# Optimization experiments

Measured on AMD Instinct MI355X. Metric: run time of the kernel, lower is better.

Reference implementation:

```python
import jax, jax.numpy as jnp
import numpy as np

B = 64        # batch
V1 = 4096     # nodes, layer 1 (D)
V2 = 1024     # nodes after pool/4
DF = 8        # input features (DFeat)
K1 = 25       # Chebyshev order layer 1
K2 = 25       # Chebyshev order layer 2
F1 = 32       # CL1_F
F2 = 64       # CL2_F
FC1F = 512    # FC1_F
FC2F = 10     # FC2_F
E1 = 65536    # nnz of L1
E2 = 16384    # nnz of L2
FC1Fin = F2 * (V1 // 16)  # 16384


def setup_inputs() -> dict:
    key = jax.random.key(0)
    ks = jax.random.split(key, 16)
    x = jax.random.normal(ks[0], (B, V1, DF), jnp.float32)
    L1_rows = jax.random.randint(ks[1], (E1,), 0, V1, dtype=jnp.int32)
    L1_cols = jax.random.randint(ks[2], (E1,), 0, V1, dtype=jnp.int32)
    # small values keep the order-25 Chebyshev recursion numerically tame
    L1_vals = jax.random.normal(ks[3], (E1,), jnp.float32) * 0.05
    L2_rows = jax.random.randint(ks[4], (E2,), 0, V2, dtype=jnp.int32)
    L2_cols = jax.random.randint(ks[5], (E2,), 0, V2, dtype=jnp.int32)
    L2_vals = jax.random.normal(ks[6], (E2,), jnp.float32) * 0.05

    def glorot(k, shape, fin, fout):
        s = np.sqrt(2.0 / (fin + fout)).astype(np.float32)
        return jax.random.uniform(k, shape, jnp.float32, -s, s)

    cl1_w = glorot(ks[7], (F1, K1 * DF), K1, F1)
    cl1_b = jnp.zeros((F1,), jnp.float32)
    cl2_w = glorot(ks[8], (F2, K2 * F1), K2 * F1, F2)
    cl2_b = jnp.zeros((F2,), jnp.float32)
    fc1_w = glorot(ks[9], (FC1F, FC1Fin), FC1Fin, FC1F)
    fc1_b = jnp.zeros((FC1F,), jnp.float32)
    fc2_w = glorot(ks[10], (FC2F, FC1F), FC1F, FC2F)
    fc2_b = jnp.zeros((FC2F,), jnp.float32)
    return dict(x=x, L1_rows=L1_rows, L1_cols=L1_cols, L1_vals=L1_vals,
                L2_rows=L2_rows, L2_cols=L2_cols, L2_vals=L2_vals,
                cl1_w=cl1_w, cl1_b=cl1_b, cl2_w=cl2_w, cl2_b=cl2_b,
                fc1_w=fc1_w, fc1_b=fc1_b, fc2_w=fc2_w, fc2_b=fc2_b)


def _cheb_conv(x, rows, cols, vals, W, b, K):
    """Chebyshev graph conv. x: [B, V, Fin]; sparse L as COO edge lists."""
    Bb, V, Fin = x.shape
    x0 = x.transpose(1, 2, 0).reshape(V, Fin * Bb)  # [V, Fin*B]

    def spmm(y):  # sparse [V,V] @ dense [V, C]
        return jax.ops.segment_sum(vals[:, None] * y[cols], rows, num_segments=V)

    x1 = spmm(x0)

    def step(carry, _):
        xm2, xm1 = carry
        xk = 2.0 * spmm(xm1) - xm2
        return (xm1, xk), xk

    _, rest = jax.lax.scan(step, (x0, x1), None, length=K - 2)
    stack = jnp.concatenate([x0[None], x1[None], rest], axis=0)  # [K, V, Fin*B]
    # [K,V,Fin,B] -> [B,V,Fin,K] -> [B*V, Fin*K], matching torch layout
    feat = stack.reshape(K, V, Fin, Bb).transpose(3, 1, 2, 0).reshape(Bb * V, Fin * K)
    out = feat @ W.T + b
    return out.reshape(Bb, V, -1)


def _max_pool(x, p):
    Bb, V, F = x.shape
    return x.reshape(Bb, V // p, p, F).max(axis=2)


def reference(x, L1_rows, L1_cols, L1_vals, L2_rows, L2_cols, L2_vals,
              cl1_w, cl1_b, cl2_w, cl2_b, fc1_w, fc1_b, fc2_w, fc2_b):
    h = _cheb_conv(x, L1_rows, L1_cols, L1_vals, cl1_w, cl1_b, K1)
    h = jax.nn.relu(h)
    h = _max_pool(h, 4)                                   # [B, V/4, F1]
    h = _cheb_conv(h, L2_rows, L2_cols, L2_vals, cl2_w, cl2_b, K2)
    h = jax.nn.relu(h)
    h = _max_pool(h, 4)                                   # [B, V/16, F2]
    h = h.reshape(-1, FC1Fin)
    h = jax.nn.relu(h @ fc1_w.T + fc1_b)
    # dropout treated as identity (eval mode / d=0)
    return h @ fc2_w.T + fc2_b                            # [B, FC2F]
```

## Files before the change

### kernel.cpp

```cpp
#include <hip/hip_runtime.h>
#include <hip/hip_fp16.h>

#define B_    64
#define V1_   4096
#define V2_   1024
#define DF_   8
#define K_    25
#define NP_   13
#define F1_   32
#define F2_   64
#define FC1F_ 512
#define FC2F_ 10
#define E1_   65536
#define E2_   16384
#define C1_   512
#define C2_   2048
#define FCIN_ 16384

typedef short bf16x8 __attribute__((ext_vector_type(8)));
typedef float f32x4  __attribute__((ext_vector_type(4)));

#define FMA_MIX_LO(acc, qv, gv) \
    asm("v_fma_mix_f32 %0, %1, %2, %0 op_sel:[1,0,0] op_sel_hi:[1,1,0]" \
        : "+v"(acc) : "v"(qv), "v"(gv))
#define FMA_MIX_HI(acc, qv, gv) \
    asm("v_fma_mix_f32 %0, %1, %2, %0 op_sel:[1,1,0] op_sel_hi:[1,1,0]" \
        : "+v"(acc) : "v"(qv), "v"(gv))

__device__ __forceinline__ unsigned short f2bf(float x) {
    unsigned u = __float_as_uint(x);
    u += 0x7FFFu + ((u >> 16) & 1u);
    return (unsigned short)(u >> 16);
}
__device__ __forceinline__ float h2f_lo(unsigned u) {
    return __half2float(__ushort_as_half((unsigned short)(u & 0xFFFFu)));
}
__device__ __forceinline__ float h2f_hi(unsigned u) {
    return __half2float(__ushort_as_half((unsigned short)(u >> 16)));
}

__global__ __launch_bounds__(256) void k_transpose_rm(const float* __restrict__ x,
                                                      unsigned* __restrict__ XP,
                                                      unsigned* __restrict__ stk0) {
    __shared__ float tsh[DF_][B_][16];
    const int t = threadIdx.x;
    const int v0 = blockIdx.x * 16;
    for (int rep = 0; rep < 4; ++rep) {
        int idx = rep*256 + t;
        int b = idx >> 4, vv = idx & 15;
        const float4* p = (const float4*)&x[((size_t)b*V1_ + v0 + vv)*DF_];
        float4 a0 = p[0], a1 = p[1];
        tsh[0][b][vv]=a0.x; tsh[1][b][vv]=a0.y; tsh[2][b][vv]=a0.z; tsh[3][b][vv]=a0.w;
        tsh[4][b][vv]=a1.x; tsh[5][b][vv]=a1.y; tsh[6][b][vv]=a1.z; tsh[7][b][vv]=a1.w;
    }
    __syncthreads();
    for (int rep = 0; rep < 16; ++rep) {
        int idx = rep*256 + t;
        int c2 = idx & 255, vv = idx >> 8;
        int c = c2*2, fin = c >> 6, b = c & 63;
        float xa = tsh[fin][b][vv], xb = tsh[fin][b+1][vv];
        __half2 hh = __floats2half2_rn(xa, xb);
        XP[(size_t)(v0+vv)*256 + c2]   = *(const unsigned*)&hh;
        stk0[(size_t)(v0+vv)*256 + c2] = (unsigned)f2bf(xa) | ((unsigned)f2bf(xb) << 16);
    }
}

__global__ __launch_bounds__(256) void k_count(const int* __restrict__ rows, int E,
                                               int* __restrict__ cnt) {
    int e = blockIdx.x*256 + threadIdx.x;
    if (e < E) atomicAdd(&cnt[rows[e]], 1);
}

__global__ __launch_bounds__(256) void k_scan(const int* __restrict__ cnt, int V,
                                              int* __restrict__ offs, int* __restrict__ cursor) {
    __shared__ int psum[256];
    int t = threadIdx.x;
    int chunk = V >> 8;
    int lo = t*chunk;
    int s = 0;
    for (int i = lo; i < lo+chunk; ++i) s += (cnt[i] + 3) & ~3;
    psum[t] = s;
    __syncthreads();
    for (int off = 1; off < 256; off <<= 1) {
        int val = (t >= off) ? psum[t-off] : 0;
        __syncthreads();
        psum[t] += val;
        __syncthreads();
    }
    int run = (t == 0) ? 0 : psum[t-1];
    for (int i = lo; i < lo+chunk; ++i) {
        offs[i] = run; cursor[i] = run;
        run += (cnt[i] + 3) & ~3;
    }
    if (t == 255) offs[V] = run;
}

__global__ __launch_bounds__(256) void k_scatter(const int* __restrict__ rows,
                                                 const int* __restrict__ cols,
                                                 const float* __restrict__ vals, int E,
                                                 int shift,
                                                 int* __restrict__ cursor,
                                                 unsigned* __restrict__ ep) {
    int e = blockIdx.x*256 + threadIdx.x;
    if (e < E) {
        int p = atomicAdd(&cursor[rows[e]], 1);
        unsigned hv = (unsigned)__half_as_ushort(__float2half(vals[e]));
        ep[p] = (hv << 16) | ((unsigned)cols[e] << shift);
    }
}

__global__ __launch_bounds__(512) void k_dcheb1(int k,
        const unsigned short* __restrict__ Xsrc,
        unsigned short* __restrict__ Xown,
        unsigned short* __restrict__ stk16,
        const int* __restrict__ offs,
        const unsigned* __restrict__ ep) {
    const int t = threadIdx.x;
    const int lane = t & 63;
    const int v = blockIdx.x*8 + (t >> 6);
    const int e0 = offs[v], e1 = offs[v+1];
    const unsigned loff = (unsigned)lane * 16u;
    float acc[8];
#pragma unroll
    for (int j = 0; j < 8; ++j) acc[j] = 0.f;
    const char* srcb = (const char*)Xsrc;

    for (int e = e0; e < e1; e += 4) {
        const uint4 q = *(const uint4*)&ep[e];
        const uint4 g0 = *(const uint4*)(srcb + ((q.x & 0xFFFFu)*1024u + loff));
        const uint4 g1 = *(const uint4*)(srcb + ((q.y & 0xFFFFu)*1024u + loff));
        const uint4 g2 = *(const uint4*)(srcb + ((q.z & 0xFFFFu)*1024u + loff));
        const uint4 g3 = *(const uint4*)(srcb + ((q.w & 0xFFFFu)*1024u + loff));
        FMA_MIX_LO(acc[0], q.x, g0.x); FMA_MIX_HI(acc[1], q.x, g0.x);
        FMA_MIX_LO(acc[2], q.x, g0.y); FMA_MIX_HI(acc[3], q.x, g0.y);
        FMA_MIX_LO(acc[4], q.x, g0.z); FMA_MIX_HI(acc[5], q.x, g0.z);
        FMA_MIX_LO(acc[6], q.x, g0.w); FMA_MIX_HI(acc[7], q.x, g0.w);
        FMA_MIX_LO(acc[0], q.y, g1.x); FMA_MIX_HI(acc[1], q.y, g1.x);
        FMA_MIX_LO(acc[2], q.y, g1.y); FMA_MIX_HI(acc[3], q.y, g1.y);
        FMA_MIX_LO(acc[4], q.y, g1.z); FMA_MIX_HI(acc[5], q.y, g1.z);
        FMA_MIX_LO(acc[6], q.y, g1.w); FMA_MIX_HI(acc[7], q.y, g1.w);
        FMA_MIX_LO(acc[0], q.z, g2.x); FMA_MIX_HI(acc[1], q.z, g2.x);
        FMA_MIX_LO(acc[2], q.z, g2.y); FMA_MIX_HI(acc[3], q.z, g2.y);
        FMA_MIX_LO(acc[4], q.z, g2.z); FMA_MIX_HI(acc[5], q.z, g2.z);
        FMA_MIX_LO(acc[6], q.z, g2.w); FMA_MIX_HI(acc[7], q.z, g2.w);
        FMA_MIX_LO(acc[0], q.w, g3.x); FMA_MIX_HI(acc[1], q.w, g3.x);
        FMA_MIX_LO(acc[2], q.w, g3.y); FMA_MIX_HI(acc[3], q.w, g3.y);
        FMA_MIX_LO(acc[4], q.w, g3.z); FMA_MIX_HI(acc[5], q.w, g3.z);
        FMA_MIX_LO(acc[6], q.w, g3.w); FMA_MIX_HI(acc[7], q.w, g3.w);
    }

    float xn[8];
    if (k > 1) {
        const uint4 old = *(const uint4*)((const char*)Xown + ((size_t)v*1024 + loff));
        xn[0] = fmaf(2.f, acc[0], -h2f_lo(old.x));
        xn[1] = fmaf(2.f, acc[1], -h2f_hi(old.x));
        xn[2] = fmaf(2.f, acc[2], -h2f_lo(old.y));
        xn[3] = fmaf(2.f, acc[3], -h2f_hi(old.y));
        xn[4] = fmaf(2.f, acc[4], -h2f_lo(old.z));
        xn[5] = fmaf(2.f, acc[5], -h2f_hi(old.z));
        xn[6] = fmaf(2.f, acc[6], -h2f_lo(old.w));
        xn[7] = fmaf(2.f, acc[7], -h2f_hi(old.w));
    } else {
#pragma unroll
        for (int j = 0; j < 8; ++j) xn[j] = acc[j];
    }

    uint4 hp;
    { __half2 h0 = __floats2half2_rn(xn[0], xn[1]); hp.x = *(const unsigned*)&h0;
      __half2 h1 = __floats2half2_rn(xn[2], xn[3]); hp.y = *(const unsigned*)&h1;
      __half2 h2 = __floats2half2_rn(xn[4], xn[5]); hp.z = *(const unsigned*)&h2;
      __half2 h3 = __floats2half2_rn(xn[6], xn[7]); hp.w = *(const unsigned*)&h3; }
    *(uint4*)((char*)Xown + ((size_t)v*1024 + loff)) = hp;

    uint4 bp;
    bp.x = (unsigned)f2bf(xn[0]) | ((unsigned)f2bf(xn[1]) << 16);
    bp.y = (unsigned)f2bf(xn[2]) | ((unsigned)f2bf(xn[3]) << 16);
    bp.z = (unsigned)f2bf(xn[4]) | ((unsigned)f2bf(xn[5]) << 16);
    bp.w = (unsigned)f2bf(xn[6]) | ((unsigned)f2bf(xn[7]) << 16);
    *(uint4*)((char*)stk16 + (((size_t)k*V1_ + v)*1024 + loff)) = bp;
}

template<int FIN, int F>
__global__ __launch_bounds__(256) void k_wprep(const float* __restrict__ W,
                                               unsigned short* __restrict__ Wb) {
    int idx = blockIdx.x*256 + threadIdx.x;
    int kk  = idx & 7;
    int f   = (idx >> 3) % F;
    int g   = (idx >> 3) / F % 4;
    int fin = idx / (8*F*4);
    int k = g*8 + kk;
    Wb[idx] = (k < K_) ? f2bf(W[(size_t)f*(FIN*K_) + fin*K_ + k]) : 0;
}

__global__ __launch_bounds__(256) void k_gemm1b(const unsigned short* __restrict__ stk16,
                                                const unsigned short* __restrict__ Wb,
                                                const float* __restrict__ bias,
                                                float* __restrict__ X0T2) {
    const int t = threadIdx.x, lane = t & 63, wave = t >> 6;
    const int v2 = blockIdx.x*4 + wave;
    const int m = lane & 15, g = lane >> 4;
    int kbase[8];
#pragma unroll
    for (int j = 0; j < 8; ++j) {
        int kq = g*8 + j; if (kq > 24) kq = 24;
        kbase[j] = kq * (V1_*C1_);
    }
    float bv[2] = { bias[m], bias[16+m] };
    f32x4 pool[4][2];

    for (int vv = 0; vv < 4; ++vv) {
        const int v = v2*4 + vv;
        f32x4 acc[4][2];
#pragma unroll
        for (int mt = 0; mt < 4; ++mt)
#pragma unroll
            for (int ft = 0; ft < 2; ++ft) acc[mt][ft] = (f32x4){0.f,0.f,0.f,0.f};

        for (int fin = 0; fin < DF_; ++fin) {
            const int cbase = v*C1_ + fin*64 + m;
            const bf16x8 bw0 = *(const bf16x8*)&Wb[((fin*4+g)*F1_ + m)*8];
            const bf16x8 bw1 = *(const bf16x8*)&Wb[((fin*4+g)*F1_ + 16 + m)*8];
#pragma unroll
            for (int mt = 0; mt < 4; ++mt) {
                unsigned short au[8];
#pragma unroll
                for (int j = 0; j < 8; ++j)
                    au[j] = stk16[(size_t)(kbase[j] + cbase + mt*16)];
                bf16x8 a;
                __builtin_memcpy(&a, au, 16);
                acc[mt][0] = __builtin_amdgcn_mfma_f32_16x16x32_bf16(a, bw0, acc[mt][0], 0,0,0);
                acc[mt][1] = __builtin_amdgcn_mfma_f32_16x16x32_bf16(a, bw1, acc[mt][1], 0,0,0);
            }
        }
#pragma unroll
        for (int mt = 0; mt < 4; ++mt)
#pragma unroll
            for (int ft = 0; ft < 2; ++ft) {
                if (vv == 0) pool[mt][ft] = acc[mt][ft];
                else {
#pragma unroll
                    for (int j = 0; j < 4; ++j)
                        pool[mt][ft][j] = fmaxf(pool[mt][ft][j], acc[mt][ft][j]);
                }
            }
    }

#pragma unroll
    for (int mt = 0; mt < 4; ++mt)
#pragma unroll
        for (int ft = 0; ft < 2; ++ft)
#pragma unroll
            for (int j = 0; j < 4; ++j) {
                float mx = fmaxf(pool[mt][ft][j] + bv[ft], 0.f);
                int b = mt*16 + g*4 + j;
                int f = ft*16 + m;
                X0T2[(size_t)(f*64+b)*V2_ + v2] = mx;
            }
}

template<int V, int THREADS, int MINW>
__global__ __launch_bounds__(THREADS, MINW) void k_cheb2(
        const float* __restrict__ X0T,
        const int* __restrict__ offs,
        const unsigned* __restrict__ ep,
        unsigned* __restrict__ stk) {
    constexpr int RPT = V / THREADS;
    __shared__ uint2 buf[2*V];
    const int c0 = blockIdx.x*4;
    const int t = threadIdx.x;
    int e0r[RPT], e1r[RPT];
    unsigned tlo[RPT][4];
    unsigned* __restrict__ pl[4];
#pragma unroll
    for (int j = 0; j < 4; ++j) pl[j] = stk + (size_t)(c0+j)*NP_*V;

#pragma unroll
    for (int r = 0; r < RPT; ++r) {
        const int v = r*THREADS + t;
        e0r[r] = offs[v]; e1r[r] = offs[v+1];
        float xj[4];
#pragma unroll
        for (int j = 0; j < 4; ++j) {
            xj[j] = X0T[(size_t)(c0+j)*V + v];
            tlo[r][j] = f2bf(xj[j]);
        }
        __half2 ha = __floats2half2_rn(xj[0], xj[1]);
        __half2 hb = __floats2half2_rn(xj[2], xj[3]);
        buf[v] = make_uint2(*(const unsigned*)&ha, *(const unsigned*)&hb);
    }
    __syncthreads();

    auto step = [&](const uint2* __restrict__ src, uint2* __restrict__ dst,
                    bool first, bool last, int plane) {
#pragma unroll
        for (int r = 0; r < RPT; ++r) {
            const int v = r*THREADS + t;
            float acc[4][4];
#pragma unroll
            for (int j = 0; j < 4; ++j)
#pragma unroll
                for (int i = 0; i < 4; ++i) acc[j][i] = 0.f;
            const int ee0 = e0r[r], ee1 = e1r[r];
            uint4 q = *(const uint4*)&ep[ee0];
            for (int e = ee0; e < ee1; e += 4) {
                const uint4 qn = *(const uint4*)&ep[e + 4];
                const uint2 g0 = *(const uint2*)((const char*)src + (q.x & 0xFFFFu));
                const uint2 g1 = *(const uint2*)((const char*)src + (q.y & 0xFFFFu));
                const uint2 g2 = *(const uint2*)((const char*)src + (q.z & 0xFFFFu));
                const uint2 g3 = *(const uint2*)((const char*)src + (q.w & 0xFFFFu));
                FMA_MIX_LO(acc[0][0], q.x, g0.x); FMA_MIX_HI(acc[1][0], q.x, g0.x);
                FMA_MIX_LO(acc[2][0], q.x, g0.y); FMA_MIX_HI(acc[3][0], q.x, g0.y);
                FMA_MIX_LO(acc[0][1], q.y, g1.x); FMA_MIX_HI(acc[1][1], q.y, g1.x);
                FMA_MIX_LO(acc[2][1], q.y, g1.y); FMA_MIX_HI(acc[3][1], q.y, g1.y);
                FMA_MIX_LO(acc[0][2], q.z, g2.x); FMA_MIX_HI(acc[1][2], q.z, g2.x);
                FMA_MIX_LO(acc[2][2], q.z, g2.y); FMA_MIX_HI(acc[3][2], q.z, g2.y);
                FMA_MIX_LO(acc[0][3], q.w, g3.x); FMA_MIX_HI(acc[1][3], q.w, g3.x);
                FMA_MIX_LO(acc[2][3], q.w, g3.y); FMA_MIX_HI(acc[3][3], q.w, g3.y);
                q = qn;
            }
            float gs[4];
#pragma unroll
            for (int j = 0; j < 4; ++j)
                gs[j] = (acc[j][0]+acc[j][1])+(acc[j][2]+acc[j][3]);
            float xn[4];
            if (first) {
#pragma unroll
                for (int j = 0; j < 4; ++j) xn[j] = gs[j];
            } else {
                const uint2 old = dst[v];
                xn[0] = fmaf(2.f, gs[0], -h2f_lo(old.x));
                xn[1] = fmaf(2.f, gs[1], -h2f_hi(old.x));
                xn[2] = fmaf(2.f, gs[2], -h2f_lo(old.y));
                xn[3] = fmaf(2.f, gs[3], -h2f_hi(old.y));
            }
            if (!last) {
                __half2 ha = __floats2half2_rn(xn[0], xn[1]);
                __half2 hb = __floats2half2_rn(xn[2], xn[3]);
                dst[v] = make_uint2(*(const unsigned*)&ha, *(const unsigned*)&hb);
            }
            unsigned h[4];
#pragma unroll
            for (int j = 0; j < 4; ++j) h[j] = f2bf(xn[j]);
            if (plane < 0) {
#pragma unroll
                for (int j = 0; j < 4; ++j) tlo[r][j] = h[j];
            } else {
#pragma unroll
                for (int j = 0; j < 4; ++j)
                    pl[j][(size_t)plane*V + v] = tlo[r][j] | (h[j] << 16);
            }
        }
        __syncthreads();
    };

    step(buf, buf + V, true, false, 0);
    for (int k = 2; k < 24; k += 2) {
        step(buf + V, buf, false, false, -1);
        step(buf, buf + V, false, false, (k + 1) >> 1);
    }
    step(buf + V, buf, false, true, -1);

#pragma unroll
    for (int r = 0; r < RPT; ++r) {
        const int v = r*THREADS + t;
#pragma unroll
        for (int j = 0; j < 4; ++j)
            pl[j][(size_t)12*V + v] = tlo[r][j];
    }
}

__global__ __launch_bounds__(256) void k_gemm2(const unsigned* __restrict__ STK,
                                               const unsigned short* __restrict__ Wb,
                                               const float* __restrict__ bias,
                                               float* __restrict__ FCINT) {
    const int t = threadIdx.x, lane = t & 63, wave = t >> 6;
    const int b = blockIdx.x;
    const int v0 = blockIdx.y*128 + wave*32;
    const int m = lane & 15, g = lane >> 4;
    int offp[4];
#pragma unroll
    for (int p = 0; p < 4; ++p) {
        int pl = 4*g + p; if (pl > 12) pl = 12;
        offp[p] = pl*V2_ + v0 + m;
    }

    f32x4 acc[2][4];
#pragma unroll
    for (int mt = 0; mt < 2; ++mt)
#pragma unroll
        for (int ft = 0; ft < 4; ++ft) acc[mt][ft] = (f32x4){0.f,0.f,0.f,0.f};

#pragma unroll 4
    for (int fin = 0; fin < F1_; ++fin) {
        const unsigned* sp = STK + (size_t)(fin*64 + b)*(NP_*V2_);
        unsigned ua[4], ub[4];
#pragma unroll
        for (int p = 0; p < 4; ++p) { ua[p] = sp[offp[p]]; ub[p] = sp[offp[p] + 16]; }
        bf16x8 a0, a1;
        __builtin_memcpy(&a0, ua, 16);
        __builtin_memcpy(&a1, ub, 16);
#pragma unroll
        for (int ft = 0; ft < 4; ++ft) {
            const bf16x8 bw = *(const bf16x8*)&Wb[((fin*4+g)*F2_ + ft*16 + m)*8];
            acc[0][ft] = __builtin_amdgcn_mfma_f32_16x16x32_bf16(a0, bw, acc[0][ft], 0,0,0);
            acc[1][ft] = __builtin_amdgcn_mfma_f32_16x16x32_bf16(a1, bw, acc[1][ft], 0,0,0);
        }
    }
#pragma unroll
    for (int mt = 0; mt < 2; ++mt)
#pragma unroll
        for (int ft = 0; ft < 4; ++ft) {
            f32x4 a = acc[mt][ft];
            float mx = fmaxf(fmaxf(a[0],a[1]), fmaxf(a[2],a[3])) + bias[ft*16 + m];
            mx = fmaxf(mx, 0.f);
            int v2 = blockIdx.y*32 + wave*8 + mt*4 + g;
            FCINT[((size_t)v2*64 + ft*16 + m)*64 + b] = mx;
        }
}

__global__ __launch_bounds__(256) void k_fc1_init(const float* __restrict__ bias,
                                                  float* __restrict__ O) {
    int idx = blockIdx.x*256 + threadIdx.x;
    O[idx] = bias[idx & (FC1F_-1)];
}

__global__ __launch_bounds__(256) void k_fc1(const float* __restrict__ AT,
                                             const float* __restrict__ W,
                                             float* __restrict__ O) {
    const int t = threadIdx.x;
    const int b = t & 63;
    const int jq = __builtin_amdgcn_readfirstlane(t >> 6);
    const int j0 = blockIdx.x*32 + jq*8;
    const int i0 = blockIdx.y*1024;
    float acc[8] = {};
    for (int i = i0; i < i0 + 1024; i += 4) {
        float a0 = AT[(size_t)(i+0)*64 + b];
        float a1 = AT[(size_t)(i+1)*64 + b];
        float a2 = AT[(size_t)(i+2)*64 + b];
        float a3 = AT[(size_t)(i+3)*64 + b];
#pragma unroll
        for (int jj = 0; jj < 8; ++jj) {
            const float* wp = &W[(size_t)(j0+jj)*FCIN_ + i];
            acc[jj] = fmaf(a0, wp[0], acc[jj]);
            acc[jj] = fmaf(a1, wp[1], acc[jj]);
            acc[jj] = fmaf(a2, wp[2], acc[jj]);
            acc[jj] = fmaf(a3, wp[3], acc[jj]);
        }
    }
#pragma unroll
    for (int jj = 0; jj < 8; ++jj)
        atomicAdd(&O[b*FC1F_ + j0 + jj], acc[jj]);
}

__global__ void k_fc2(const float* __restrict__ O1, const float* __restrict__ W2,
                      const float* __restrict__ b2, float* __restrict__ out) {
    int c = blockIdx.x;
    int b = threadIdx.x;
    float s = b2[c];
    for (int j = 0; j < FC1F_; ++j)
        s = fmaf(fmaxf(O1[b*FC1F_ + j], 0.f), W2[c*FC1F_ + j], s);
    out[b*FC2F_ + c] = s;
}

extern "C" void kernel_launch(void* const* d_in, const int* in_sizes, int n_in,
                              void* d_out, int out_size, void* d_ws, size_t ws_size,
                              hipStream_t stream) {
    const float* x   = (const float*)d_in[0];
    const int*   l1r = (const int*)d_in[1];
    const int*   l1c = (const int*)d_in[2];
    const float* l1v = (const float*)d_in[3];
    const int*   l2r = (const int*)d_in[4];
    const int*   l2c = (const int*)d_in[5];
    const float* l2v = (const float*)d_in[6];
    const float* w1  = (const float*)d_in[7];
    const float* b1  = (const float*)d_in[8];
    const float* w2  = (const float*)d_in[9];
    const float* b2  = (const float*)d_in[10];
    const float* fw1 = (const float*)d_in[11];
    const float* fb1 = (const float*)d_in[12];
    const float* fw2 = (const float*)d_in[13];
    const float* fb2 = (const float*)d_in[14];
    float* out = (float*)d_out;

    char* wsp = (char*)d_ws;
    size_t off = 0;
    auto alloc = [&](size_t bytes) -> void* {
        void* p = wsp + off;
        off += (bytes + 255) & ~size_t(255);
        return p;
    };
    void*     STKU  = alloc((size_t)C2_*NP_*V2_*4);
    unsigned short* stk16 = (unsigned short*)STKU;
    unsigned*       STACK = (unsigned*)STKU;
    unsigned short* XB0   = (unsigned short*)alloc((size_t)V1_*C1_*2);
    unsigned short* XB1   = (unsigned short*)alloc((size_t)V1_*C1_*2);
    float*    X0T2  = (float*)alloc((size_t)C2_*V2_*4);
    float*    FCINT = (float*)alloc((size_t)FCIN_*B_*4);
    float*    FC1O  = (float*)alloc((size_t)B_*FC1F_*4);
    unsigned short* WB1 = (unsigned short*)alloc((size_t)DF_*4*F1_*8*2);
    unsigned short* WB2 = (unsigned short*)alloc((size_t)F1_*4*F2_*8*2);
    int*      cnt1  = (int*)alloc(V1_*4);
    int*      offs1 = (int*)alloc((V1_+1)*4);
    int*      cur1  = (int*)alloc(V1_*4);
    unsigned* ep1   = (unsigned*)alloc((size_t)(E1_ + 4*V1_ + 8)*4);
    int*      cnt2  = (int*)alloc(V2_*4);
    int*      offs2 = (int*)alloc((V2_+1)*4);
    int*      cur2  = (int*)alloc(V2_*4);
    unsigned* ep2   = (unsigned*)alloc((size_t)(E2_ + 4*V2_ + 8)*4);

    hipMemsetAsync(cnt1, 0, V1_*4, stream);
    hipMemsetAsync(ep1, 0, (size_t)(E1_ + 4*V1_ + 8)*4, stream);
    hipMemsetAsync(cnt2, 0, V2_*4, stream);
    hipMemsetAsync(ep2, 0, (size_t)(E2_ + 4*V2_ + 8)*4, stream);
    hipLaunchKernelGGL(k_count,   dim3(E1_/256), dim3(256), 0, stream, l1r, E1_, cnt1);
    hipLaunchKernelGGL(k_scan,    dim3(1),       dim3(256), 0, stream, cnt1, V1_, offs1, cur1);
    hipLaunchKernelGGL(k_scatter, dim3(E1_/256), dim3(256), 0, stream, l1r, l1c, l1v, E1_, 0, cur1, ep1);
    hipLaunchKernelGGL(k_count,   dim3(E2_/256), dim3(256), 0, stream, l2r, E2_, cnt2);
    hipLaunchKernelGGL(k_scan,    dim3(1),       dim3(256), 0, stream, cnt2, V2_, offs2, cur2);
    hipLaunchKernelGGL(k_scatter, dim3(E2_/256), dim3(256), 0, stream, l2r, l2c, l2v, E2_, 3, cur2, ep2);
    hipLaunchKernelGGL((k_wprep<DF_,F1_>), dim3(DF_*4*F1_*8/256), dim3(256), 0, stream, w1, WB1);
    hipLaunchKernelGGL((k_wprep<F1_,F2_>), dim3(F1_*4*F2_*8/256), dim3(256), 0, stream, w2, WB2);

    hipLaunchKernelGGL(k_transpose_rm, dim3(V1_/16), dim3(256), 0, stream,
                       x, (unsigned*)XB0, (unsigned*)stk16);
    for (int k = 1; k <= 24; ++k) {
        unsigned short* src = (k & 1) ? XB0 : XB1;
        unsigned short* own = (k & 1) ? XB1 : XB0;
        hipLaunchKernelGGL(k_dcheb1, dim3(V1_/8), dim3(512), 0, stream,
                           k, src, own, stk16, offs1, ep1);
    }
    hipLaunchKernelGGL(k_gemm1b, dim3(V2_/4), dim3(256), 0, stream, stk16, WB1, b1, X0T2);

    hipLaunchKernelGGL((k_cheb2<V2_,512,4>), dim3(C2_/4), dim3(512), 0, stream,
                       X0T2, offs2, ep2, STACK);
    hipLaunchKernelGGL(k_gemm2, dim3(64, 8), dim3(256), 0, stream, STACK, WB2, b2, FCINT);

    hipLaunchKernelGGL(k_fc1_init, dim3(B_*FC1F_/256), dim3(256), 0, stream, fb1, FC1O);
    hipLaunchKernelGGL(k_fc1, dim3(16, 16), dim3(256), 0, stream, FCINT, fw1, FC1O);
    hipLaunchKernelGGL(k_fc2, dim3(FC2F_), dim3(B_), 0, stream, FC1O, fw2, fb2, out);
}
```

Baseline: 630.1 us.

## Run FC1 on bf16 MFMA with bf16 activations and pre-converted weights

Replaces the scalar fp32 FMA FC1 kernel with a bf16 MFMA 16x16x32 kernel. gemm2 now writes its pooled activations as bf16 in batch-major layout, and a new prep kernel converts the 512x16384 fc1 weight to bf16 on every call. The aim is to cut the FMA-bound FC1 cost and halve activation traffic. In exchange it adds a full read and write pass over the 32MB fp32 weight each call and lowers FC1 to bf16 precision.

```diff
diff --git a/kernel.cpp b/kernel.cpp
--- a/kernel.cpp
+++ b/kernel.cpp
@@ -192,6 +192,15 @@
     Wb[idx] = (k < K_) ? f2bf(W[(size_t)f*(FIN*K_) + fin*K_ + k]) : 0;
 }
 
+__global__ __launch_bounds__(256) void k_wprep_fc(const float* __restrict__ W,
+                                                  unsigned short* __restrict__ Wb) {
+    int idx = (blockIdx.x*256 + threadIdx.x)*4;
+    float4 w = *(const float4*)&W[idx];
+    ushort4 o;
+    o.x = f2bf(w.x); o.y = f2bf(w.y); o.z = f2bf(w.z); o.w = f2bf(w.w);
+    *(ushort4*)&Wb[idx] = o;
+}
+
 __global__ __launch_bounds__(256) void k_gemm1b(const unsigned short* __restrict__ stk16,
                                                 const unsigned short* __restrict__ Wb,
                                                 const float* __restrict__ bias,
@@ -372,7 +381,7 @@
 __global__ __launch_bounds__(256) void k_gemm2(const unsigned* __restrict__ STK,
                                                const unsigned short* __restrict__ Wb,
                                                const float* __restrict__ bias,
-                                               float* __restrict__ FCINT) {
+                                               unsigned short* __restrict__ ABF) {
     const int t = threadIdx.x, lane = t & 63, wave = t >> 6;
     const int b = blockIdx.x;
     const int v0 = blockIdx.y*128 + wave*32;
@@ -414,7 +423,7 @@
             float mx = fmaxf(fmaxf(a[0],a[1]), fmaxf(a[2],a[3])) + bias[ft*16 + m];
             mx = fmaxf(mx, 0.f);
             int v2 = blockIdx.y*32 + wave*8 + mt*4 + g;
-            FCINT[((size_t)v2*64 + ft*16 + m)*64 + b] = mx;
+            ABF[(size_t)b*FCIN_ + v2*64 + ft*16 + m] = f2bf(mx);
         }
 }
 
@@ -424,32 +433,24 @@
     O[idx] = bias[idx & (FC1F_-1)];
 }
 
-__global__ __launch_bounds__(256) void k_fc1(const float* __restrict__ AT,
-                                             const float* __restrict__ W,
-                                             float* __restrict__ O) {
-    const int t = threadIdx.x;
-    const int b = t & 63;
-    const int jq = __builtin_amdgcn_readfirstlane(t >> 6);
-    const int j0 = blockIdx.x*32 + jq*8;
-    const int i0 = blockIdx.y*1024;
-    float acc[8] = {};
-    for (int i = i0; i < i0 + 1024; i += 4) {
-        float a0 = AT[(size_t)(i+0)*64 + b];
-        float a1 = AT[(size_t)(i+1)*64 + b];
-        float a2 = AT[(size_t)(i+2)*64 + b];
-        float a3 = AT[(size_t)(i+3)*64 + b];
-#pragma unroll
-        for (int jj = 0; jj < 8; ++jj) {
-            const float* wp = &W[(size_t)(j0+jj)*FCIN_ + i];
-            acc[jj] = fmaf(a0, wp[0], acc[jj]);
-            acc[jj] = fmaf(a1, wp[1], acc[jj]);
-            acc[jj] = fmaf(a2, wp[2], acc[jj]);
-            acc[jj] = fmaf(a3, wp[3], acc[jj]);
-        }
-    }
-#pragma unroll
-    for (int jj = 0; jj < 8; ++jj)
-        atomicAdd(&O[b*FC1F_ + j0 + jj], acc[jj]);
+__global__ __launch_bounds__(256) void k_fc1m(const unsigned short* __restrict__ ABF,
+                                              const unsigned short* __restrict__ WBF,
+                                              float* __restrict__ O) {
+    const int t = threadIdx.x, lane = t & 63, wave = t >> 6;
+    const int j0 = blockIdx.x*16;
+    const int k0 = blockIdx.y*1024;
+    const int m = lane & 15, g = lane >> 4;
+    const int m0 = wave*16;
+    f32x4 acc = (f32x4){0.f,0.f,0.f,0.f};
+#pragma unroll 4
+    for (int k = k0; k < k0+1024; k += 32) {
+        const bf16x8 a = *(const bf16x8*)&ABF[(size_t)(m0+m)*FCIN_ + k + g*8];
+        const bf16x8 w = *(const bf16x8*)&WBF[(size_t)(j0+m)*FCIN_ + k + g*8];
+        acc = __builtin_amdgcn_mfma_f32_16x16x32_bf16(a, w, acc, 0,0,0);
+    }
+#pragma unroll
+    for (int r = 0; r < 4; ++r)
+        atomicAdd(&O[(size_t)(m0 + g*4 + r)*FC1F_ + j0 + m], acc[r]);
 }
 
 __global__ void k_fc2(const float* __restrict__ O1, const float* __restrict__ W2,
@@ -495,7 +496,8 @@
     unsigned short* XB0   = (unsigned short*)alloc((size_t)V1_*C1_*2);
     unsigned short* XB1   = (unsigned short*)alloc((size_t)V1_*C1_*2);
     float*    X0T2  = (float*)alloc((size_t)C2_*V2_*4);
-    float*    FCINT = (float*)alloc((size_t)FCIN_*B_*4);
+    unsigned short* ABF = (unsigned short*)alloc((size_t)B_*FCIN_*2);
+    unsigned short* WBF = (unsigned short*)alloc((size_t)FC1F_*FCIN_*2);
     float*    FC1O  = (float*)alloc((size_t)B_*FC1F_*4);
     unsigned short* WB1 = (unsigned short*)alloc((size_t)DF_*4*F1_*8*2);
     unsigned short* WB2 = (unsigned short*)alloc((size_t)F1_*4*F2_*8*2);
@@ -520,6 +522,7 @@
     hipLaunchKernelGGL(k_scatter, dim3(E2_/256), dim3(256), 0, stream, l2r, l2c, l2v, E2_, 3, cur2, ep2);
     hipLaunchKernelGGL((k_wprep<DF_,F1_>), dim3(DF_*4*F1_*8/256), dim3(256), 0, stream, w1, WB1);
     hipLaunchKernelGGL((k_wprep<F1_,F2_>), dim3(F1_*4*F2_*8/256), dim3(256), 0, stream, w2, WB2);
+    hipLaunchKernelGGL(k_wprep_fc, dim3(FC1F_*FCIN_/1024), dim3(256), 0, stream, fw1, WBF);
 
     hipLaunchKernelGGL(k_transpose_rm, dim3(V1_/16), dim3(256), 0, stream,
                        x, (unsigned*)XB0, (unsigned*)stk16);
@@ -533,9 +536,9 @@
 
     hipLaunchKernelGGL((k_cheb2<V2_,512,4>), dim3(C2_/4), dim3(512), 0, stream,
                        X0T2, offs2, ep2, STACK);
-    hipLaunchKernelGGL(k_gemm2, dim3(64, 8), dim3(256), 0, stream, STACK, WB2, b2, FCINT);
+    hipLaunchKernelGGL(k_gemm2, dim3(64, 8), dim3(256), 0, stream, STACK, WB2, b2, ABF);
 
     hipLaunchKernelGGL(k_fc1_init, dim3(B_*FC1F_/256), dim3(256), 0, stream, fb1, FC1O);
-    hipLaunchKernelGGL(k_fc1, dim3(16, 16), dim3(256), 0, stream, FCINT, fw1, FC1O);
+    hipLaunchKernelGGL(k_fc1m, dim3(32, 16), dim3(256), 0, stream, ABF, WBF, FC1O);
     hipLaunchKernelGGL(k_fc2, dim3(FC2F_), dim3(B_), 0, stream, FC1O, fw2, fb2, out);
 }
```

Result: faster. 520.8 us (-17.3%).
